# Kernel tuning notes

Measured on AMD Instinct MI355X. Metric: run time of the kernel, lower is better.

The kernel has to match this reference:

```python
import jax, jax.numpy as jnp
import numpy as np

B, T, F, C, D, R = 8, 1000, 96, 16, 64, 4
S = F // R
EPS = 1e-5


def _ln(x, g, b):
    # LayerNorm over last (frequency) dim, matching nn.LayerNorm(fe) on [B,C,T,F]
    m = jnp.mean(x, -1, keepdims=True)
    v = jnp.mean((x - m) ** 2, -1, keepdims=True)
    return (x - m) / jnp.sqrt(v + EPS) * g + b


def _gelu(x):
    return jax.nn.gelu(x, approximate=False)  # torch nn.GELU default (erf)


def setup_inputs() -> dict:
    key = jax.random.key(0)
    ks = jax.random.split(key, 16)
    def nrm(k, shape, fan_in):
        return jax.random.normal(k, shape, jnp.float32) / np.sqrt(fan_in)
    return {
        "input": jax.random.normal(ks[0], (B, 2, T, F), jnp.float32),
        "ln_in_g": jnp.ones((F,), jnp.float32),
        "ln_in_b": jnp.zeros((F,), jnp.float32),
        "w_in": nrm(ks[1], (C, 2), 2),
        "b_in": jnp.zeros((C,), jnp.float32),
        "gru_wx": nrm(ks[2], (3 * C, C), C),   # z|r|n input projections (1x1 conv, no bias)
        "gru_wh": nrm(ks[3], (3 * C, C), C),   # z|r|n hidden projections
        "ln_att_g": jnp.ones((F,), jnp.float32),
        "ln_att_b": jnp.zeros((F,), jnp.float32),
        "wq": nrm(ks[4], (D, C), C),
        "bq": jnp.zeros((D,), jnp.float32),
        "wk": nrm(ks[5], (D, C), C),
        "bk": jnp.zeros((D,), jnp.float32),
        "wv": nrm(ks[6], (D, C), C),
        "bv": jnp.zeros((D,), jnp.float32),
        "wo": nrm(ks[7], (C, D), D),
        "bo": jnp.zeros((C,), jnp.float32),
        "ln_m_g": jnp.ones((F,), jnp.float32),
        "ln_m_b": jnp.zeros((F,), jnp.float32),
        "w_m1": nrm(ks[8], (C, C), C),
        "b_m1": jnp.zeros((C,), jnp.float32),
        "w_m2": nrm(ks[9], (C, C), C),
        "b_m2": jnp.zeros((C,), jnp.float32),
        "ln_out_g": jnp.ones((F,), jnp.float32),
        "ln_out_b": jnp.zeros((F,), jnp.float32),
        "w_out": nrm(ks[10], (2, C), C),
        "b_out": jnp.zeros((2,), jnp.float32),
    }


def _fwd(input, ln_in_g, ln_in_b, w_in, b_in, gru_wx, gru_wh,
         ln_att_g, ln_att_b, wq, bq, wk, bk, wv, bv, wo, bo,
         ln_m_g, ln_m_b, w_m1, b_m1, w_m2, b_m2,
         ln_out_g, ln_out_b, w_out, b_out):
    b = input.shape[0]
    # conv_in: LayerNorm -> 1x1 Conv (2->C) -> GELU
    x = _gelu(jnp.einsum('oc,bctf->botf', w_in, _ln(input, ln_in_g, ln_in_b))
              + b_in[None, :, None, None])  # [B,C,T,F]

    # ConvGRU (kernel 1, no bias): precompute input gates, scan over time
    gx = jnp.einsum('gc,bctf->tbgf', gru_wx, x)  # [T,B,3C,F]
    h0 = jnp.zeros((b, C, F), x.dtype)

    def step(h, gx_t):
        gh = jnp.einsum('gc,bcf->bgf', gru_wh, h)
        zx, rx, nx = jnp.split(gx_t, 3, axis=1)
        zh, rh, nh = jnp.split(gh, 3, axis=1)
        z = jax.nn.sigmoid(zx + zh)
        r = jax.nn.sigmoid(rx + rh)
        n = jnp.tanh(nx + r * nh)
        h = (1.0 - z) * n + z * h
        return h, h

    h_last, hs = jax.lax.scan(step, h0, gx)
    x = x + jnp.moveaxis(hs, 0, 2)  # residual add of GRU output

    # PreNormShortcut(LongShortAttention): local window r + segment-pooled long keys over F
    y = _ln(x, ln_att_g, ln_att_b)
    q = jnp.einsum('dc,bctf->btfd', wq, y) + bq
    k = jnp.einsum('dc,bctf->btfd', wk, y) + bk
    v = jnp.einsum('dc,bctf->btfd', wv, y) + bv
    qs = q.reshape(b, T, S, R, D)
    kk = k.reshape(b, T, S, R, D)
    vv = v.reshape(b, T, S, R, D)
    k_long = kk.mean(3)  # [B,T,S,D]
    v_long = vv.mean(3)
    scale = D ** -0.5
    sc_s = jnp.einsum('btsqd,btskd->btsqk', qs, kk) * scale   # local scores [B,T,S,R,R]
    sc_l = jnp.einsum('btsqd,btmd->btsqm', qs, k_long) * scale  # long scores [B,T,S,R,S]
    a = jax.nn.softmax(jnp.concatenate([sc_s, sc_l], -1), axis=-1)
    o = (jnp.einsum('btsqk,btskd->btsqd', a[..., :R], vv)
         + jnp.einsum('btsqm,btmd->btsqd', a[..., R:], v_long))
    o = o.reshape(b, T, F, D)
    x = x + jnp.einsum('cd,btfd->bctf', wo, o) + bo[None, :, None, None]

    # PreNormShortcut(conv-GELU-conv)
    y = _ln(x, ln_m_g, ln_m_b)
    y = _gelu(jnp.einsum('oc,bctf->botf', w_m1, y) + b_m1[None, :, None, None])
    y = jnp.einsum('oc,bctf->botf', w_m2, y) + b_m2[None, :, None, None]
    x = x + y

    # conv_out: LayerNorm -> 1x1 Conv (C->2) -> Tanh, then outer residual
    y = jnp.tanh(jnp.einsum('oc,bctf->botf', w_out, _ln(x, ln_out_g, ln_out_b))
                 + b_out[None, :, None, None])
    return input + y, h_last


def reference(input, ln_in_g, ln_in_b, w_in, b_in, gru_wx, gru_wh,
              ln_att_g, ln_att_b, wq, bq, wk, bk, wv, bv, wo, bo,
              ln_m_g, ln_m_b, w_m1, b_m1, w_m2, b_m2,
              ln_out_g, ln_out_b, w_out, b_out):
    return _fwd(input, ln_in_g, ln_in_b, w_in, b_in, gru_wx, gru_wh,
                ln_att_g, ln_att_b, wq, bq, wk, bk, wv, bv, wo, bo,
                ln_m_g, ln_m_b, w_m1, b_m1, w_m2, b_m2,
                ln_out_g, ln_out_b, w_out, b_out)
```

## Files before the change

### kernel.cpp

```cpp
#include <hip/hip_runtime.h>
#include <math.h>

#define B_ 8
#define T_ 1000
#define F_ 96
#define C_ 16
#define D_ 64
#define EPS_ 1e-5f
#define CH_ 40

typedef short bfrag8 __attribute__((ext_vector_type(8)));
typedef float facc4 __attribute__((ext_vector_type(4)));
typedef float f2v __attribute__((ext_vector_type(2)));
#define MFMA16 __builtin_amdgcn_mfma_f32_16x16x32_bf16

__device__ __forceinline__ float gelu_erf(float v){
    return 0.5f*v*(1.0f+erff(v*0.70710678118654752440f));
}
__device__ __forceinline__ float dot4(float4 a, float4 b){
    return a.x*b.x + a.y*b.y + a.z*b.z + a.w*b.w;
}
__device__ __forceinline__ float ex2(float x){
    float r; asm("v_exp_f32 %0, %1" : "=v"(r) : "v"(x)); return r;
}
__device__ __forceinline__ float ex2n(float x){
    float r; asm("v_exp_f32 %0, -%1" : "=v"(r) : "v"(x)); return r;
}
__device__ __forceinline__ unsigned short f2bf(float x){
    unsigned int u = __float_as_uint(x);
    return (unsigned short)((u + 0x7fffu + ((u>>16)&1u)) >> 16);
}
__device__ __forceinline__ float bf2f(unsigned short s){
    return __uint_as_float(((unsigned int)s)<<16);
}
__device__ __forceinline__ unsigned int pack2bf(float a, float b){
    return (unsigned int)f2bf(a) | ((unsigned int)f2bf(b)<<16);
}

__global__ __launch_bounds__(128) void k_conv_in(
    const float* __restrict__ in, const float* __restrict__ g, const float* __restrict__ bb,
    const float* __restrict__ w_in, const float* __restrict__ b_in,
    float* __restrict__ x,
    const float* __restrict__ wq, const float* __restrict__ bq,
    const float* __restrict__ wk, const float* __restrict__ bk,
    const float* __restrict__ wv, const float* __restrict__ wo,
    const float* __restrict__ wm1, const float* __restrict__ wm2,
    short* __restrict__ gtb, float* __restrict__ uvw,
    short* __restrict__ wv_bf, short* __restrict__ wo_bf,
    short* __restrict__ wm1_bf, short* __restrict__ wm2_bf)
{
    int bt = blockIdx.x;
    int tid = threadIdx.x;

    if (bt == B_*T_){
        for (int idx = tid; idx < 256; idx += 128){
            int c1 = idx & 15, c2 = idx >> 4;
            float acc = 0.f;
            #pragma unroll 8
            for (int d=0; d<64; ++d)
                acc += wq[d*16 + c1] * wk[d*16 + c2];
            gtb[c2*16 + c1] = (short)f2bf(0.125f * acc);
        }
        if (tid < 16){
            float a = 0.f;
            for (int d=0; d<64; ++d) a += wq[d*16 + tid] * bk[d];
            uvw[tid] = 0.125f * a;
        } else if (tid < 32){
            int cc = tid - 16;
            float a = 0.f;
            for (int d=0; d<64; ++d) a += bq[d] * wk[d*16 + cc];
            uvw[16 + cc] = 0.125f * a;
        } else if (tid == 32){
            float a = 0.f;
            for (int d=0; d<64; ++d) a += bq[d] * bk[d];
            uvw[32] = 0.125f * a;
        }
        for (int i = tid; i < 1024; i += 128){
            wv_bf[i] = (short)f2bf(wv[i]);
            wo_bf[i] = (short)f2bf(wo[i]);
        }
        for (int i = tid; i < 256; i += 128){
            wm1_bf[i] = (short)f2bf(wm1[i]);
            wm2_bf[i] = (short)f2bf(wm2[i]);
        }
        return;
    }

    int b = bt / T_; int t = bt % T_;
    float i0=0.f, i1=0.f;
    size_t base0 = ((size_t)(b*2+0)*T_ + t)*F_;
    size_t base1 = ((size_t)(b*2+1)*T_ + t)*F_;
    if (tid < F_){ i0 = in[base0+tid]; i1 = in[base1+tid]; }
    float s0=i0, q0=i0*i0, s1=i1, q1=i1*i1;
    #pragma unroll
    for (int off=32; off>=1; off>>=1){
        s0 += __shfl_xor(s0, off);
        q0 += __shfl_xor(q0, off);
        s1 += __shfl_xor(s1, off);
        q1 += __shfl_xor(q1, off);
    }
    __shared__ float part[2][4];
    if ((tid & 63) == 0){
        float* p = part[tid>>6];
        p[0]=s0; p[1]=q0; p[2]=s1; p[3]=q1;
    }
    __syncthreads();
    float S0 = part[0][0]+part[1][0];
    float Q0 = part[0][1]+part[1][1];
    float S1 = part[0][2]+part[1][2];
    float Q1 = part[0][3]+part[1][3];
    float m0 = S0*(1.f/F_), m1 = S1*(1.f/F_);
    float ri0 = rsqrtf(Q0*(1.f/F_) - m0*m0 + EPS_);
    float ri1 = rsqrtf(Q1*(1.f/F_) - m1*m1 + EPS_);
    if (tid < F_){
        float gg = g[tid], b0 = bb[tid];
        float y0 = (i0-m0)*ri0*gg + b0;
        float y1 = (i1-m1)*ri1*gg + b0;
        float xv[16];
        #pragma unroll
        for (int c=0;c<C_;++c){
            xv[c] = gelu_erf(w_in[c*2+0]*y0 + w_in[c*2+1]*y1 + b_in[c]);
        }
        float4* xp = (float4*)(x + (((size_t)b*T_+t)*F_ + tid)*C_);
        xp[0] = make_float4(xv[0],xv[1],xv[2],xv[3]);
        xp[1] = make_float4(xv[4],xv[5],xv[6],xv[7]);
        xp[2] = make_float4(xv[8],xv[9],xv[10],xv[11]);
        xp[3] = make_float4(xv[12],xv[13],xv[14],xv[15]);
    }
}

#define DPPF(src, ctrl) __int_as_float(__builtin_amdgcn_update_dpp(0, __float_as_int(src), (ctrl), 0xF, 0xF, false))
#define L2E_ 1.44269504088896340736f

#define GATHER_PAIRDOTS(XV, WZ, WR, WN, SZ, SR, SN) { \
    f2v A0,P2,P7,P5,PF,PD,P8,PA; \
    A0.x = (XV);            A0.y = DPPF((XV),0xB1); \
    P2.x = DPPF(A0.x,0x4E); P2.y = DPPF(A0.y,0x4E); \
    P7.x = DPPF(A0.x,0x141);P7.y = DPPF(A0.y,0x141); \
    P5.x = DPPF(P7.x,0x4E); P5.y = DPPF(P7.y,0x4E); \
    PF.x = DPPF(A0.x,0x140);PF.y = DPPF(A0.y,0x140); \
    PD.x = DPPF(PF.x,0x4E); PD.y = DPPF(PF.y,0x4E); \
    P8.x = DPPF(PF.x,0x141);P8.y = DPPF(PF.y,0x141); \
    PA.x = DPPF(P8.x,0x4E); PA.y = DPPF(P8.y,0x4E); \
    f2v sza = WZ[0]*A0, sra = WR[0]*A0, sna = WN[0]*A0; \
    sza = __builtin_elementwise_fma(WZ[1],P2,sza); \
    sra = __builtin_elementwise_fma(WR[1],P2,sra); \
    sna = __builtin_elementwise_fma(WN[1],P2,sna); \
    sza = __builtin_elementwise_fma(WZ[2],P7,sza); \
    sra = __builtin_elementwise_fma(WR[2],P7,sra); \
    sna = __builtin_elementwise_fma(WN[2],P7,sna); \
    sza = __builtin_elementwise_fma(WZ[3],P5,sza); \
    sra = __builtin_elementwise_fma(WR[3],P5,sra); \
    sna = __builtin_elementwise_fma(WN[3],P5,sna); \
    f2v szb = WZ[4]*PF, srb = WR[4]*PF, snb = WN[4]*PF; \
    szb = __builtin_elementwise_fma(WZ[5],PD,szb); \
    srb = __builtin_elementwise_fma(WR[5],PD,srb); \
    snb = __builtin_elementwise_fma(WN[5],PD,snb); \
    szb = __builtin_elementwise_fma(WZ[6],P8,szb); \
    srb = __builtin_elementwise_fma(WR[6],P8,srb); \
    snb = __builtin_elementwise_fma(WN[6],P8,snb); \
    szb = __builtin_elementwise_fma(WZ[7],PA,szb); \
    srb = __builtin_elementwise_fma(WR[7],PA,srb); \
    snb = __builtin_elementwise_fma(WN[7],PA,snb); \
    SZ = sza + szb; SR = sra + srb; SN = sna + snb; \
}

__global__ __launch_bounds__(256, 1) void k_gru(
    const float* __restrict__ x, const float* __restrict__ wx, const float* __restrict__ wh,
    float* __restrict__ hs, float* __restrict__ d_out)
{
    int blk = blockIdx.x;
    int b = blk / 24, f0 = (blk % 24) * 4;
    int tid = threadIdx.x;
    int wave = tid >> 6, lane = tid & 63;
    int c = lane & 15, ch = lane >> 4;
    int f = f0 + ch;

    __shared__ float GG[2][(CH_+1)*192];

    const int pm0[8] = {0,2,7,5,15,13,8,10};
    const int pm1[8] = {1,3,6,4,14,12,9,11};

    if (wave != 0){
        float4 Wxz[4], Wxr[4], Wxn[4];
        #pragma unroll
        for (int q=0;q<4;++q){
            float4 az = *(const float4*)(wx + ( 0+c)*16 + 4*q);
            float4 ar = *(const float4*)(wx + (16+c)*16 + 4*q);
            float4 an = *(const float4*)(wx + (32+c)*16 + 4*q);
            Wxz[q] = make_float4(az.x*L2E_, az.y*L2E_, az.z*L2E_, az.w*L2E_);
            Wxr[q] = make_float4(ar.x*L2E_, ar.y*L2E_, ar.z*L2E_, ar.w*L2E_);
            Wxn[q] = make_float4(an.x*2.f*L2E_, an.y*2.f*L2E_, an.z*2.f*L2E_, an.w*2.f*L2E_);
        }
        const float* gb0 = x + (size_t)b*T_*(F_*C_) + f*C_;
        const int tl0 = (wave-1)*14;
        const int tl1 = (tl0 + 14 < CH_) ? tl0 + 14 : CH_;
        #define PRODUCE(K, BF) { \
            _Pragma("unroll 2") \
            for (int tl=tl0; tl<tl1; ++tl){ \
                const float* xp2 = gb0 + (size_t)((K)*CH_ + tl)*(F_*C_); \
                float4 x0 = *(const float4*)(xp2 + 0); \
                float4 x1 = *(const float4*)(xp2 + 4); \
                float4 x2 = *(const float4*)(xp2 + 8); \
                float4 x3 = *(const float4*)(xp2 + 12); \
                float zx = dot4(Wxz[0],x0)+dot4(Wxz[1],x1)+dot4(Wxz[2],x2)+dot4(Wxz[3],x3); \
                float rx = dot4(Wxr[0],x0)+dot4(Wxr[1],x1)+dot4(Wxr[2],x2)+dot4(Wxr[3],x3); \
                float nx = dot4(Wxn[0],x0)+dot4(Wxn[1],x1)+dot4(Wxn[2],x2)+dot4(Wxn[3],x3); \
                float* gq = &GG[BF][tl*192 + lane]; \
                gq[0] = zx; gq[64] = rx; gq[128] = nx; \
            } }
        PRODUCE(0, 0);
        __syncthreads();
        for (int k=0; k<T_/CH_; ++k){
            if (k+1 < T_/CH_){
                if ((k+1)&1){ PRODUCE(k+1, 1); } else { PRODUCE(k+1, 0); }
            }
            __syncthreads();
        }
        #undef PRODUCE
    } else {
        __builtin_amdgcn_s_setprio(1);
        f2v Wz[8], Wr[8], Wn[8];
        #pragma unroll
        for (int j=0;j<8;++j){
            int ka = c ^ pm0[j], kb = c ^ pm1[j];
            Wz[j].x = L2E_*wh[( 0+c)*16 + ka];      Wz[j].y = L2E_*wh[( 0+c)*16 + kb];
            Wr[j].x = L2E_*wh[(16+c)*16 + ka];      Wr[j].y = L2E_*wh[(16+c)*16 + kb];
            Wn[j].x = 2.f*L2E_*wh[(32+c)*16 + ka];  Wn[j].y = 2.f*L2E_*wh[(32+c)*16 + kb];
        }
        float hc = 0.f;
        size_t hsb = (size_t)b*T_*(F_*C_) + f0*C_ + lane;
        __syncthreads();
        for (int k=0; k<T_/CH_; ++k){
            const float* gp = GG[k&1];
            float gzv = gp[lane], grv = gp[64+lane], gnv = gp[128+lane];
            #pragma unroll 8
            for (int tl=0; tl<CH_; ++tl){
                const float* np = gp + (tl+1)*192 + lane;
                float gzn = np[0], grn = np[64], gnn = np[128];
                f2v SZ, SR, SN;
                GATHER_PAIRDOTS(hc, Wz, Wr, Wn, SZ, SR, SN);
                float z = __builtin_amdgcn_rcpf(1.f + ex2n(gzv + (SZ.x + SZ.y)));
                float r = __builtin_amdgcn_rcpf(1.f + ex2n(grv + (SR.x + SR.y)));
                float u = __builtin_amdgcn_rcpf(1.f + ex2(fmaf(r, SN.x + SN.y, gnv)));
                float n = fmaf(-2.f, u, 1.f);
                hc = n + z*(hc - n);
                hs[hsb + (size_t)(k*CH_ + tl)*(F_*C_)] = hc;
                gzv = gzn; grv = grn; gnv = gnn;
            }
            __syncthreads();
        }
        d_out[(size_t)B_*2*T_*F_ + ((size_t)b*C_ + c)*F_ + f] = hc;
    }
}

#define XR_FL   0
#define YB_SH   3072
#define YGB_SH  5376
#define PG_SH   3072
#define YMB_SH  7680
#define E_FL    4224
#define GL_FL   4320
#define GM_FL   4416
#define VBT_SH  8880
#define VLBT_SH 15024
#define SC_FL   8536
#define OB_SH   17072
#define PL_SH   23216
#define GTB_SH  17072
#define UU_FL   8728
#define VV_FL   8744
#define W0_FL   8760
#define OSC_FL  8776
#define MEA_FL  9288
#define RST_FL  9304
#define TOTF    13144

__device__ __forceinline__ void ln_stats16(float* S, int tid){
    int c = tid & 15, g = tid >> 4;
    float s=0.f, q=0.f;
    #pragma unroll
    for (int i=0;i<6;++i){
        float v = S[XR_FL + (g*6+i)*16 + c];
        s += v; q += v*v;
    }
    S[OSC_FL + g*16 + c] = s;
    S[OSC_FL + 256 + g*16 + c] = q;
    __syncthreads();
    if (tid < 16){
        float Sm=0.f, Q=0.f;
        #pragma unroll
        for (int g2=0; g2<16; ++g2){
            Sm += S[OSC_FL + g2*16 + tid];
            Q  += S[OSC_FL + 256 + g2*16 + tid];
        }
        float m = Sm*(1.f/96.f);
        S[MEA_FL+tid] = m;
        S[RST_FL+tid] = rsqrtf(Q*(1.f/96.f) - m*m + EPS_);
    }
    __syncthreads();
}

__global__ __launch_bounds__(256) void k_tail(
    const float* __restrict__ x, const float* __restrict__ hs, const float* __restrict__ input,
    const float* __restrict__ ln_att_g, const float* __restrict__ ln_att_b,
    const short* __restrict__ gtb, const float* __restrict__ uvw,
    const short* __restrict__ wv_bf, const float* __restrict__ bv,
    const short* __restrict__ wo_bf, const float* __restrict__ bo,
    const float* __restrict__ ln_m_g, const float* __restrict__ ln_m_b,
    const short* __restrict__ wm1_bf, const float* __restrict__ bm1,
    const short* __restrict__ wm2_bf, const float* __restrict__ bm2,
    const float* __restrict__ ln_o_g, const float* __restrict__ ln_o_b,
    const float* __restrict__ w_out, const float* __restrict__ b_out,
    float* __restrict__ out)
{
    int bt = blockIdx.x; int b = bt / T_; int t = bt % T_;
    int tid = threadIdx.x;
    int w = tid >> 6, lane = tid & 63;
    int n = lane & 15, q2 = lane >> 4;
    __shared__ float S[TOTF];
    short* Ssh = (short*)S;
    const bfrag8 ZF = {0,0,0,0,0,0,0,0};
    const int svl = (n >> 1) & 3;
    const int swo = n & 7;

    size_t xbase = ((size_t)b*T_ + t)*(size_t)(F_*C_);

    {
        const float4* xg = (const float4*)(x + xbase);
        const float4* hg = (const float4*)(hs + xbase);
        float4* XR4 = (float4*)(S + XR_FL);
        for (int i4 = tid; i4 < 384; i4 += 256){
            float4 a = xg[i4], h = hg[i4];
            XR4[i4] = make_float4(a.x+h.x, a.y+h.y, a.z+h.z, a.w+h.w);
        }
        if (tid < 64){
            int cc2 = tid >> 2, c1g = (tid & 3)*4;
            *(uint2*)(Ssh + GTB_SH + cc2*24 + c1g) = *(const uint2*)(gtb + cc2*16 + c1g);
        } else if (tid < 97){
            S[UU_FL + (tid - 64)] = uvw[tid - 64];
        }
    }
    bfrag8 Bv = ZF, Bm1 = ZF, Bm2 = ZF;
    if (q2 < 2){
        Bv  = *(const bfrag8*)(wv_bf  + (16*w + n)*16 + q2*8);
        Bm1 = *(const bfrag8*)(wm1_bf + n*16 + q2*8);
        Bm2 = *(const bfrag8*)(wm2_bf + n*16 + q2*8);
    }
    bfrag8 Bo0 = *(const bfrag8*)(wo_bf + n*64 + q2*8);
    bfrag8 Bo1 = *(const bfrag8*)(wo_bf + n*64 + 32 + q2*8);
    float bvr  = bv[16*w + n];
    float bor  = bo[n];
    float bm1r = bm1[n];
    float bm2r = bm2[n];
    __syncthreads();

    ln_stats16(S, tid);

    {
        float4* XR4 = (float4*)(S + XR_FL);
        for (int i4 = tid; i4 < 384; i4 += 256){
            int f = i4 >> 2, c4 = i4 & 3;
            float4 v = XR4[i4];
            float4 m4 = *(float4*)(S + MEA_FL + 4*c4);
            float4 r4 = *(float4*)(S + RST_FL + 4*c4);
            float gg = ln_att_g[f], b2 = ln_att_b[f];
            float y0 = (v.x - m4.x)*r4.x*gg + b2;
            float y1 = (v.y - m4.y)*r4.y*gg + b2;
            float y2 = (v.z - m4.z)*r4.z*gg + b2;
            float y3 = (v.w - m4.w)*r4.w*gg + b2;
            uint2 pk = make_uint2(pack2bf(y0,y1), pack2bf(y2,y3));
            *(uint2*)(Ssh + YB_SH + f*24 + c4*4) = pk;
        }
    }
    __syncthreads();

    if (tid < 96){
        int f = tid;
        float yv[16];
        uint4 u0 = *(const uint4*)(Ssh + YB_SH + f*24);
        uint4 u1 = *(const uint4*)(Ssh + YB_SH + f*24 + 8);
        unsigned int uu[8] = {u0.x,u0.y,u0.z,u0.w,u1.x,u1.y,u1.z,u1.w};
        #pragma unroll
        for (int j=0;j<8;++j){
            yv[2*j]   = bf2f((unsigned short)(uu[j] & 0xffff));
            yv[2*j+1] = bf2f((unsigned short)(uu[j] >> 16));
        }
        float de = 0.f, dg = 0.f;
        #pragma unroll
        for (int cc=0; cc<16; ++cc){
            de += yv[cc]*S[UU_FL+cc];
            dg += yv[cc]*S[VV_FL+cc];
        }
        S[E_FL + f]  = de + S[W0_FL];
        S[GL_FL + f] = dg;
    }
    for (int e = tid; e < 384; e += 256){
        int m = e >> 4, cc = e & 15;
        float sm = bf2f((unsigned short)Ssh[YB_SH + (4*m+0)*24 + cc])
                 + bf2f((unsigned short)Ssh[YB_SH + (4*m+1)*24 + cc])
                 + bf2f((unsigned short)Ssh[YB_SH + (4*m+2)*24 + cc])
                 + bf2f((unsigned short)Ssh[YB_SH + (4*m+3)*24 + cc]);
        Ssh[YMB_SH + m*24 + cc] = (short)f2bf(0.25f*sm);
    }
    if (tid < 128){
        int row = 24 + (tid >> 4), cc = tid & 15;
        Ssh[YMB_SH + row*24 + cc] = 0;
    }
    __syncthreads();

    {
        #pragma unroll
        for (int mt=0; mt<6; ++mt){
            bfrag8 A = ZF;
            if (q2 < 2) A = *(const bfrag8*)(Ssh + YB_SH + (mt*16 + n)*24 + q2*8);
            facc4 acc = {bvr, bvr, bvr, bvr};
            acc = MFMA16(A, Bv, acc, 0, 0, 0);
            uint2 pk = make_uint2(pack2bf(acc[0],acc[1]), pack2bf(acc[2],acc[3]));
            int g = 2*mt + (q2>>1);
            *(uint2*)(Ssh + VBT_SH + (16*w + n)*96 + ((g^svl)<<3) + ((q2&1)<<2)) = pk;
        }
        #pragma unroll
        for (int mt=0; mt<2; ++mt){
            bfrag8 A = ZF;
            if (q2 < 2) A = *(const bfrag8*)(Ssh + YMB_SH + (mt*16 + n)*24 + q2*8);
            facc4 acc = {bvr, bvr, bvr, bvr};
            acc = MFMA16(A, Bv, acc, 0, 0, 0);
            uint2 pk = make_uint2(pack2bf(acc[0],acc[1]), pack2bf(acc[2],acc[3]));
            int g = 2*mt + (q2>>1);
            *(uint2*)(Ssh + VLBT_SH + (16*w + n)*32 + ((g^svl)<<3) + ((q2&1)<<2)) = pk;
        }
        bfrag8 Bg = ZF;
        if (q2 < 2) Bg = *(const bfrag8*)(Ssh + GTB_SH + n*24 + q2*8);
        for (int mt = w; mt < 6; mt += 4){
            bfrag8 A = ZF;
            if (q2 < 2) A = *(const bfrag8*)(Ssh + YB_SH + (mt*16 + n)*24 + q2*8);
            facc4 acc = {0.f,0.f,0.f,0.f};
            acc = MFMA16(A, Bg, acc, 0, 0, 0);
            #pragma unroll
            for (int r=0;r<4;++r)
                Ssh[YGB_SH + (mt*16 + q2*4 + r)*24 + n] = (short)f2bf(acc[r]);
        }
        if (tid >= 224 && tid < 248){
            int m = tid - 224;
            float a2 = 0.f;
            #pragma unroll
            for (int cc=0; cc<16; ++cc)
                a2 += bf2f((unsigned short)Ssh[YMB_SH + m*24 + cc]) * S[VV_FL + cc];
            S[GM_FL + m] = a2;
        }
    }
    __syncthreads();

    for (int j = w; j < 18; j += 4){
        int mt = j / 3, kind = j % 3;
        bfrag8 A = ZF;
        if (q2 < 2) A = *(const bfrag8*)(Ssh + YGB_SH + (mt*16 + n)*24 + q2*8);
        bfrag8 Bf = ZF;
        if (kind == 0){
            if (q2 < 2) Bf = *(const bfrag8*)(Ssh + YB_SH + (mt*16 + n)*24 + q2*8);
        } else {
            int nt = kind - 1;
            if (q2 < 2) Bf = *(const bfrag8*)(Ssh + YMB_SH + (nt*16 + n)*24 + q2*8);
        }
        facc4 acc = {0.f,0.f,0.f,0.f};
        acc = MFMA16(A, Bf, acc, 0, 0, 0);
        if (kind == 0){
            if ((n >> 2) == q2){
                #pragma unroll
                for (int r=0;r<4;++r)
                    S[SC_FL + (mt*16 + q2*4 + r)*29 + (n & 3)] = acc[r];
            }
        } else {
            int nt = kind - 1;
            if (!(nt == 1 && n >= 8)){
                #pragma unroll
                for (int r=0;r<4;++r)
                    S[SC_FL + (mt*16 + q2*4 + r)*29 + 4 + nt*16 + n] = acc[r];
            }
        }
    }
    __syncthreads();

    if (tid < 96){
        int f = tid;
        int lsq = (f >> 2) & 3;
        float e_ = S[E_FL + f];
        const float* row = S + SC_FL + f*29;
        float sl[4];
        #pragma unroll
        for (int j=0;j<4;++j)
            sl[j] = row[j] + e_ + S[GL_FL + (f & ~3) + j];
        float sg[24];
        #pragma unroll
        for (int m=0;m<24;++m)
            sg[m] = row[4 + m] + e_ + S[GM_FL + m];
        float mx = sl[0];
        #pragma unroll
        for (int j=1;j<4;++j) mx = fmaxf(mx, sl[j]);
        #pragma unroll
        for (int m=0;m<24;++m) mx = fmaxf(mx, sg[m]);
        float sum = 0.f;
        #pragma unroll
        for (int j=0;j<4;++j){ sl[j] = __expf(sl[j]-mx); sum += sl[j]; }
        #pragma unroll
        for (int m=0;m<24;++m){ sg[m] = __expf(sg[m]-mx); sum += sg[m]; }
        float inv = __builtin_amdgcn_rcpf(sum);
        unsigned int lo = pack2bf(sl[0]*inv, sl[1]*inv);
        unsigned int hi = pack2bf(sl[2]*inv, sl[3]*inv);
        uint4 z4 = make_uint4(0u,0u,0u,0u);
        uint4 p0 = make_uint4(lsq==0?lo:0u, lsq==0?hi:0u, lsq==1?lo:0u, lsq==1?hi:0u);
        uint4 p1 = make_uint4(lsq==2?lo:0u, lsq==2?hi:0u, lsq==3?lo:0u, lsq==3?hi:0u);
        uint4* plp = (uint4*)(Ssh + PL_SH + f*32);
        int swp = (f >> 1) & 3;
        plp[0^swp] = p0; plp[1^swp] = p1; plp[2^swp] = z4; plp[3^swp] = z4;
        unsigned int gdw[12];
        #pragma unroll
        for (int m=0;m<12;++m) gdw[m] = pack2bf(sg[2*m]*inv, sg[2*m+1]*inv);
        uint4* pgp = (uint4*)(Ssh + PG_SH + f*48);
        pgp[0] = make_uint4(gdw[0],gdw[1],gdw[2],gdw[3]);
        pgp[1] = make_uint4(gdw[4],gdw[5],gdw[6],gdw[7]);
        pgp[2] = make_uint4(gdw[8],gdw[9],gdw[10],gdw[11]);
        pgp[3] = z4;
    }
    __syncthreads();

    {
        bfrag8 Avl = *(const bfrag8*)(Ssh + VLBT_SH + (16*w + n)*32 + ((q2^svl)<<3));
        #pragma unroll
        for (int nt=0; nt<6; ++nt){
            bfrag8 Avb = *(const bfrag8*)(Ssh + VBT_SH + (16*w + n)*96 + (((2*nt + q2)^svl)<<3));
            bfrag8 Bpl = *(const bfrag8*)(Ssh + PL_SH + (nt*16 + n)*32 + ((q2^svl)<<3));
            bfrag8 Bpg = *(const bfrag8*)(Ssh + PG_SH + (nt*16 + n)*48 + q2*8);
            facc4 acc = {0.f,0.f,0.f,0.f};
            acc = MFMA16(Avb, Bpl, acc, 0, 0, 0);
            acc = MFMA16(Avl, Bpg, acc, 0, 0, 0);
            uint2 pk = make_uint2(pack2bf(acc[0],acc[1]), pack2bf(acc[2],acc[3]));
            int go = 2*w + (q2>>1);
            *(uint2*)(Ssh + OB_SH + (nt*16 + n)*64 + ((go^swo)<<3) + ((q2&1)<<2)) = pk;
        }
    }
    __syncthreads();

    for (int mt = w; mt < 6; mt += 4){
        bfrag8 A0 = *(const bfrag8*)(Ssh + OB_SH + (mt*16 + n)*64 + ((q2^swo)<<3));
        bfrag8 A1 = *(const bfrag8*)(Ssh + OB_SH + (mt*16 + n)*64 + (((4+q2)^swo)<<3));
        facc4 acc = {bor, bor, bor, bor};
        acc = MFMA16(A0, Bo0, acc, 0, 0, 0);
        acc = MFMA16(A1, Bo1, acc, 0, 0, 0);
        #pragma unroll
        for (int r=0;r<4;++r)
            S[XR_FL + (mt*16 + q2*4 + r)*16 + n] += acc[r];
    }
    __syncthreads();

    ln_stats16(S, tid);
    {
        float4* XR4 = (float4*)(S + XR_FL);
        for (int i4 = tid; i4 < 384; i4 += 256){
            int f = i4 >> 2, c4 = i4 & 3;
            float4 v = XR4[i4];
            float4 m4 = *(float4*)(S + MEA_FL + 4*c4);
            float4 r4 = *(float4*)(S + RST_FL + 4*c4);
            float gg = ln_m_g[f], b2 = ln_m_b[f];
            float y0 = (v.x - m4.x)*r4.x*gg + b2;
            float y1 = (v.y - m4.y)*r4.y*gg + b2;
            float y2 = (v.z - m4.z)*r4.z*gg + b2;
            float y3 = (v.w - m4.w)*r4.w*gg + b2;
            uint2 pk = make_uint2(pack2bf(y0,y1), pack2bf(y2,y3));
            *(uint2*)(Ssh + YB_SH + f*24 + c4*4) = pk;
        }
    }
    __syncthreads();
    for (int mt = w; mt < 6; mt += 4){
        bfrag8 A = ZF;
        if (q2 < 2) A = *(const bfrag8*)(Ssh + YB_SH + (mt*16 + n)*24 + q2*8);
        facc4 acc = {bm1r, bm1r, bm1r, bm1r};
        acc = MFMA16(A, Bm1, acc, 0, 0, 0);
        #pragma unroll
        for (int r=0;r<4;++r)
            Ssh[YGB_SH + (mt*16 + q2*4 + r)*24 + n] = (short)f2bf(gelu_erf(acc[r]));
    }
    __syncthreads();
    for (int mt = w; mt < 6; mt += 4){
        bfrag8 A = ZF;
        if (q2 < 2) A = *(const bfrag8*)(Ssh + YGB_SH + (mt*16 + n)*24 + q2*8);
        facc4 acc = {bm2r, bm2r, bm2r, bm2r};
        acc = MFMA16(A, Bm2, acc, 0, 0, 0);
        #pragma unroll
        for (int r=0;r<4;++r)
            S[XR_FL + (mt*16 + q2*4 + r)*16 + n] += acc[r];
    }
    __syncthreads();

    ln_stats16(S, tid);
    if (tid < 192){
        int ch = tid >= 96, f = tid - 96*ch;
        float gg = ln_o_g[f], b2 = ln_o_b[f];
        float acc = b_out[ch];
        float4* XR4 = (float4*)(S + XR_FL);
        #pragma unroll
        for (int c4=0;c4<4;++c4){
            float4 x4 = XR4[f*4 + c4];
            float4 m4 = *(float4*)(S + MEA_FL + 4*c4);
            float4 r4 = *(float4*)(S + RST_FL + 4*c4);
            float4 w4 = *(const float4*)(w_out + ch*16 + 4*c4);
            float4 tm;
            tm.x = (x4.x - m4.x)*r4.x*gg + b2;
            tm.y = (x4.y - m4.y)*r4.y*gg + b2;
            tm.z = (x4.z - m4.z)*r4.z*gg + b2;
            tm.w = (x4.w - m4.w)*r4.w*gg + b2;
            acc += dot4(w4, tm);
        }
        size_t oidx = ((size_t)(b*2+ch)*T_ + t)*F_ + f;
        out[oidx] = input[oidx] + tanhf(acc);
    }
}

extern "C" void kernel_launch(void* const* d_in, const int* in_sizes, int n_in,
                              void* d_out, int out_size, void* d_ws, size_t ws_size,
                              hipStream_t stream)
{
    const float* input   = (const float*)d_in[0];
    const float* ln_in_g = (const float*)d_in[1];
    const float* ln_in_b = (const float*)d_in[2];
    const float* w_in    = (const float*)d_in[3];
    const float* b_in    = (const float*)d_in[4];
    const float* gru_wx  = (const float*)d_in[5];
    const float* gru_wh  = (const float*)d_in[6];
    const float* ln_att_g= (const float*)d_in[7];
    const float* ln_att_b= (const float*)d_in[8];
    const float* wq = (const float*)d_in[9];
    const float* bq = (const float*)d_in[10];
    const float* wk = (const float*)d_in[11];
    const float* bk = (const float*)d_in[12];
    const float* wv = (const float*)d_in[13];
    const float* bv = (const float*)d_in[14];
    const float* wo = (const float*)d_in[15];
    const float* bo = (const float*)d_in[16];
    const float* ln_m_g = (const float*)d_in[17];
    const float* ln_m_b = (const float*)d_in[18];
    const float* w_m1 = (const float*)d_in[19];
    const float* b_m1 = (const float*)d_in[20];
    const float* w_m2 = (const float*)d_in[21];
    const float* b_m2 = (const float*)d_in[22];
    const float* ln_out_g = (const float*)d_in[23];
    const float* ln_out_b = (const float*)d_in[24];
    const float* w_out = (const float*)d_in[25];
    const float* b_out = (const float*)d_in[26];
    float* out = (float*)d_out;

    const size_t NX = (size_t)B_*T_*F_*C_;
    float* x   = (float*)d_ws;
    float* hs  = x + NX;
    float* uvw = x + 2*NX;
    short* wv_bf  = (short*)(x + 2*NX + 64);
    short* wo_bf  = wv_bf + 1024;
    short* wm1_bf = wo_bf + 1024;
    short* wm2_bf = wm1_bf + 256;
    short* gtb    = wm2_bf + 256;

    k_conv_in<<<B_*T_ + 1, 128, 0, stream>>>(input, ln_in_g, ln_in_b, w_in, b_in, x,
        wq, bq, wk, bk, wv, wo, w_m1, w_m2,
        gtb, uvw, wv_bf, wo_bf, wm1_bf, wm2_bf);
    k_gru<<<192, 256, 0, stream>>>(x, gru_wx, gru_wh, hs, out);
    k_tail<<<B_*T_, 256, 0, stream>>>(x, hs, input, ln_att_g, ln_att_b,
        gtb, uvw, wv_bf, bv, wo_bf, bo, ln_m_g, ln_m_b, wm1_bf, b_m1, wm2_bf, b_m2,
        ln_out_g, ln_out_b, w_out, b_out, out);
}
```

Measured before the change: 430.5 us.

## Fuse GRU and tail kernels into time-quartered launches overlapping recurrence with tail

Merges the GRU recurrence and the per-timestep tail into one kernel, launched in four time quarters. Each launch runs 192 GRU blocks for the next quarter next to tail blocks for the previous quarter, so the serial recurrence overlaps the parallel tail work. The GRU hidden state is carried between launches through a workspace buffer, and the chunk size shrinks so it reuses the tail's shared memory. The costs are extra launches, a workspace read and write of the state, and GRU blocks competing with tail blocks for compute units. Ordering depends on the stream serialising the launches.

```diff
diff --git a/kernel.cpp b/kernel.cpp
--- a/kernel.cpp
+++ b/kernel.cpp
@@ -7,7 +7,9 @@
 #define C_ 16
 #define D_ 64
 #define EPS_ 1e-5f
-#define CH_ 40
+#define CH_ 25
+#define QT_ 250
+#define NKC_ 10
 
 typedef short bfrag8 __attribute__((ext_vector_type(8)));
 typedef float facc4 __attribute__((ext_vector_type(4)));
@@ -131,6 +133,7 @@
 
 #define DPPF(src, ctrl) __int_as_float(__builtin_amdgcn_update_dpp(0, __float_as_int(src), (ctrl), 0xF, 0xF, false))
 #define L2E_ 1.44269504088896340736f
+#define GGROW ((CH_+1)*192)
 
 #define GATHER_PAIRDOTS(XV, WZ, WR, WN, SZ, SR, SN) { \
     f2v A0,P2,P7,P5,PF,PD,P8,PA; \
@@ -165,95 +168,6 @@
     SZ = sza + szb; SR = sra + srb; SN = sna + snb; \
 }
 
-__global__ __launch_bounds__(256, 1) void k_gru(
-    const float* __restrict__ x, const float* __restrict__ wx, const float* __restrict__ wh,
-    float* __restrict__ hs, float* __restrict__ d_out)
-{
-    int blk = blockIdx.x;
-    int b = blk / 24, f0 = (blk % 24) * 4;
-    int tid = threadIdx.x;
-    int wave = tid >> 6, lane = tid & 63;
-    int c = lane & 15, ch = lane >> 4;
-    int f = f0 + ch;
-
-    __shared__ float GG[2][(CH_+1)*192];
-
-    const int pm0[8] = {0,2,7,5,15,13,8,10};
-    const int pm1[8] = {1,3,6,4,14,12,9,11};
-
-    if (wave != 0){
-        float4 Wxz[4], Wxr[4], Wxn[4];
-        #pragma unroll
-        for (int q=0;q<4;++q){
-            float4 az = *(const float4*)(wx + ( 0+c)*16 + 4*q);
-            float4 ar = *(const float4*)(wx + (16+c)*16 + 4*q);
-            float4 an = *(const float4*)(wx + (32+c)*16 + 4*q);
-            Wxz[q] = make_float4(az.x*L2E_, az.y*L2E_, az.z*L2E_, az.w*L2E_);
-            Wxr[q] = make_float4(ar.x*L2E_, ar.y*L2E_, ar.z*L2E_, ar.w*L2E_);
-            Wxn[q] = make_float4(an.x*2.f*L2E_, an.y*2.f*L2E_, an.z*2.f*L2E_, an.w*2.f*L2E_);
-        }
-        const float* gb0 = x + (size_t)b*T_*(F_*C_) + f*C_;
-        const int tl0 = (wave-1)*14;
-        const int tl1 = (tl0 + 14 < CH_) ? tl0 + 14 : CH_;
-        #define PRODUCE(K, BF) { \
-            _Pragma("unroll 2") \
-            for (int tl=tl0; tl<tl1; ++tl){ \
-                const float* xp2 = gb0 + (size_t)((K)*CH_ + tl)*(F_*C_); \
-                float4 x0 = *(const float4*)(xp2 + 0); \
-                float4 x1 = *(const float4*)(xp2 + 4); \
-                float4 x2 = *(const float4*)(xp2 + 8); \
-                float4 x3 = *(const float4*)(xp2 + 12); \
-                float zx = dot4(Wxz[0],x0)+dot4(Wxz[1],x1)+dot4(Wxz[2],x2)+dot4(Wxz[3],x3); \
-                float rx = dot4(Wxr[0],x0)+dot4(Wxr[1],x1)+dot4(Wxr[2],x2)+dot4(Wxr[3],x3); \
-                float nx = dot4(Wxn[0],x0)+dot4(Wxn[1],x1)+dot4(Wxn[2],x2)+dot4(Wxn[3],x3); \
-                float* gq = &GG[BF][tl*192 + lane]; \
-                gq[0] = zx; gq[64] = rx; gq[128] = nx; \
-            } }
-        PRODUCE(0, 0);
-        __syncthreads();
-        for (int k=0; k<T_/CH_; ++k){
-            if (k+1 < T_/CH_){
-                if ((k+1)&1){ PRODUCE(k+1, 1); } else { PRODUCE(k+1, 0); }
-            }
-            __syncthreads();
-        }
-        #undef PRODUCE
-    } else {
-        __builtin_amdgcn_s_setprio(1);
-        f2v Wz[8], Wr[8], Wn[8];
-        #pragma unroll
-        for (int j=0;j<8;++j){
-            int ka = c ^ pm0[j], kb = c ^ pm1[j];
-            Wz[j].x = L2E_*wh[( 0+c)*16 + ka];      Wz[j].y = L2E_*wh[( 0+c)*16 + kb];
-            Wr[j].x = L2E_*wh[(16+c)*16 + ka];      Wr[j].y = L2E_*wh[(16+c)*16 + kb];
-            Wn[j].x = 2.f*L2E_*wh[(32+c)*16 + ka];  Wn[j].y = 2.f*L2E_*wh[(32+c)*16 + kb];
-        }
-        float hc = 0.f;
-        size_t hsb = (size_t)b*T_*(F_*C_) + f0*C_ + lane;
-        __syncthreads();
-        for (int k=0; k<T_/CH_; ++k){
-            const float* gp = GG[k&1];
-            float gzv = gp[lane], grv = gp[64+lane], gnv = gp[128+lane];
-            #pragma unroll 8
-            for (int tl=0; tl<CH_; ++tl){
-                const float* np = gp + (tl+1)*192 + lane;
-                float gzn = np[0], grn = np[64], gnn = np[128];
-                f2v SZ, SR, SN;
-                GATHER_PAIRDOTS(hc, Wz, Wr, Wn, SZ, SR, SN);
-                float z = __builtin_amdgcn_rcpf(1.f + ex2n(gzv + (SZ.x + SZ.y)));
-                float r = __builtin_amdgcn_rcpf(1.f + ex2n(grv + (SR.x + SR.y)));
-                float u = __builtin_amdgcn_rcpf(1.f + ex2(fmaf(r, SN.x + SN.y, gnv)));
-                float n = fmaf(-2.f, u, 1.f);
-                hc = n + z*(hc - n);
-                hs[hsb + (size_t)(k*CH_ + tl)*(F_*C_)] = hc;
-                gzv = gzn; grv = grn; gnv = gnn;
-            }
-            __syncthreads();
-        }
-        d_out[(size_t)B_*2*T_*F_ + ((size_t)b*C_ + c)*F_ + f] = hc;
-    }
-}
-
 #define XR_FL   0
 #define YB_SH   3072
 #define YGB_SH  5376
@@ -301,8 +215,10 @@
     __syncthreads();
 }
 
-__global__ __launch_bounds__(256) void k_tail(
-    const float* __restrict__ x, const float* __restrict__ hs, const float* __restrict__ input,
+__global__ __launch_bounds__(256, 1) void k_mid(
+    const float* __restrict__ x, const float* __restrict__ wx, const float* __restrict__ wh,
+    float* __restrict__ hs, float* __restrict__ hstate, float* __restrict__ d_out,
+    const float* __restrict__ input,
     const float* __restrict__ ln_att_g, const float* __restrict__ ln_att_b,
     const short* __restrict__ gtb, const float* __restrict__ uvw,
     const short* __restrict__ wv_bf, const float* __restrict__ bv,
@@ -312,13 +228,107 @@
     const short* __restrict__ wm2_bf, const float* __restrict__ bm2,
     const float* __restrict__ ln_o_g, const float* __restrict__ ln_o_b,
     const float* __restrict__ w_out, const float* __restrict__ b_out,
-    float* __restrict__ out)
+    float* __restrict__ out,
+    int gru_t0, int gru_on, int tail_t0, int tail_nt)
 {
-    int bt = blockIdx.x; int b = bt / T_; int t = bt % T_;
+    __shared__ float S[TOTF];
     int tid = threadIdx.x;
+    int nGru = gru_on ? 192 : 0;
+
+    if ((int)blockIdx.x < nGru){
+        float* GG0 = S;
+        float* GG1 = S + GGROW;
+        int blk = blockIdx.x;
+        int b = blk / 24, f0 = (blk % 24) * 4;
+        int wave = tid >> 6, lane = tid & 63;
+        int c = lane & 15, ch = lane >> 4;
+        int f = f0 + ch;
+        const int k0 = gru_t0 / CH_;
+
+        const int pm0[8] = {0,2,7,5,15,13,8,10};
+        const int pm1[8] = {1,3,6,4,14,12,9,11};
+
+        if (wave != 0){
+            float4 Wxz[4], Wxr[4], Wxn[4];
+            #pragma unroll
+            for (int q=0;q<4;++q){
+                float4 az = *(const float4*)(wx + ( 0+c)*16 + 4*q);
+                float4 ar = *(const float4*)(wx + (16+c)*16 + 4*q);
+                float4 an = *(const float4*)(wx + (32+c)*16 + 4*q);
+                Wxz[q] = make_float4(az.x*L2E_, az.y*L2E_, az.z*L2E_, az.w*L2E_);
+                Wxr[q] = make_float4(ar.x*L2E_, ar.y*L2E_, ar.z*L2E_, ar.w*L2E_);
+                Wxn[q] = make_float4(an.x*2.f*L2E_, an.y*2.f*L2E_, an.z*2.f*L2E_, an.w*2.f*L2E_);
+            }
+            const float* gb0 = x + (size_t)b*T_*(F_*C_) + f*C_;
+            const int tl0 = (wave-1)*9;
+            const int tl1 = (tl0 + 9 < CH_) ? tl0 + 9 : CH_;
+            #define PRODUCE(K, GP) { \
+                _Pragma("unroll 3") \
+                for (int tl=tl0; tl<tl1; ++tl){ \
+                    const float* xp2 = gb0 + (size_t)((K)*CH_ + tl)*(F_*C_); \
+                    float4 x0 = *(const float4*)(xp2 + 0); \
+                    float4 x1 = *(const float4*)(xp2 + 4); \
+                    float4 x2 = *(const float4*)(xp2 + 8); \
+                    float4 x3 = *(const float4*)(xp2 + 12); \
+                    float zx = dot4(Wxz[0],x0)+dot4(Wxz[1],x1)+dot4(Wxz[2],x2)+dot4(Wxz[3],x3); \
+                    float rx = dot4(Wxr[0],x0)+dot4(Wxr[1],x1)+dot4(Wxr[2],x2)+dot4(Wxr[3],x3); \
+                    float nx = dot4(Wxn[0],x0)+dot4(Wxn[1],x1)+dot4(Wxn[2],x2)+dot4(Wxn[3],x3); \
+                    float* gq = (GP) + tl*192 + lane; \
+                    gq[0] = zx; gq[64] = rx; gq[128] = nx; \
+                } }
+            PRODUCE(k0, GG0);
+            __syncthreads();
+            for (int kk=0; kk<NKC_; ++kk){
+                if (kk+1 < NKC_){
+                    if ((kk+1)&1){ PRODUCE(k0+kk+1, GG1); } else { PRODUCE(k0+kk+1, GG0); }
+                }
+                __syncthreads();
+            }
+            #undef PRODUCE
+        } else {
+            __builtin_amdgcn_s_setprio(1);
+            f2v Wz[8], Wr[8], Wn[8];
+            #pragma unroll
+            for (int j=0;j<8;++j){
+                int ka = c ^ pm0[j], kb = c ^ pm1[j];
+                Wz[j].x = L2E_*wh[( 0+c)*16 + ka];      Wz[j].y = L2E_*wh[( 0+c)*16 + kb];
+                Wr[j].x = L2E_*wh[(16+c)*16 + ka];      Wr[j].y = L2E_*wh[(16+c)*16 + kb];
+                Wn[j].x = 2.f*L2E_*wh[(32+c)*16 + ka];  Wn[j].y = 2.f*L2E_*wh[(32+c)*16 + kb];
+            }
+            float hc = (gru_t0 == 0) ? 0.f : hstate[blk*64 + lane];
+            size_t hsb = (size_t)b*T_*(F_*C_) + f0*C_ + lane;
+            __syncthreads();
+            for (int kk=0; kk<NKC_; ++kk){
+                const float* gp = (kk&1) ? GG1 : GG0;
+                float gzv = gp[lane], grv = gp[64+lane], gnv = gp[128+lane];
+                #pragma unroll 5
+                for (int tl=0; tl<CH_; ++tl){
+                    const float* np = gp + (tl+1)*192 + lane;
+                    float gzn = np[0], grn = np[64], gnn = np[128];
+                    f2v SZ, SR, SN;
+                    GATHER_PAIRDOTS(hc, Wz, Wr, Wn, SZ, SR, SN);
+                    float z = __builtin_amdgcn_rcpf(1.f + ex2n(gzv + (SZ.x + SZ.y)));
+                    float r = __builtin_amdgcn_rcpf(1.f + ex2n(grv + (SR.x + SR.y)));
+                    float u = __builtin_amdgcn_rcpf(1.f + ex2(fmaf(r, SN.x + SN.y, gnv)));
+                    float n = fmaf(-2.f, u, 1.f);
+                    hc = n + z*(hc - n);
+                    hs[hsb + (size_t)((k0+kk)*CH_ + tl)*(F_*C_)] = hc;
+                    gzv = gzn; grv = grn; gnv = gnn;
+                }
+                __syncthreads();
+            }
+            hstate[blk*64 + lane] = hc;
+            if (gru_t0 + QT_ == T_)
+                d_out[(size_t)B_*2*T_*F_ + ((size_t)b*C_ + c)*F_ + f] = hc;
+        }
+        return;
+    }
+
+    int idx = blockIdx.x - nGru;
+    int b = idx / tail_nt;
+    int t = tail_t0 + idx % tail_nt;
     int w = tid >> 6, lane = tid & 63;
     int n = lane & 15, q2 = lane >> 4;
-    __shared__ float S[TOTF];
     short* Ssh = (short*)S;
     const bfrag8 ZF = {0,0,0,0,0,0,0,0};
     const int svl = (n >> 1) & 3;
@@ -659,12 +669,19 @@
     short* wm1_bf = wo_bf + 1024;
     short* wm2_bf = wm1_bf + 256;
     short* gtb    = wm2_bf + 256;
+    float* hstate = (float*)(gtb + 256);
 
     k_conv_in<<<B_*T_ + 1, 128, 0, stream>>>(input, ln_in_g, ln_in_b, w_in, b_in, x,
         wq, bq, wk, bk, wv, wo, w_m1, w_m2,
         gtb, uvw, wv_bf, wo_bf, wm1_bf, wm2_bf);
-    k_gru<<<192, 256, 0, stream>>>(x, gru_wx, gru_wh, hs, out);
-    k_tail<<<B_*T_, 256, 0, stream>>>(x, hs, input, ln_att_g, ln_att_b,
-        gtb, uvw, wv_bf, bv, wo_bf, bo, ln_m_g, ln_m_b, wm1_bf, b_m1, wm2_bf, b_m2,
-        ln_out_g, ln_out_b, w_out, b_out, out);
-}
+
+    #define MIDARGS x, gru_wx, gru_wh, hs, hstate, out, input, ln_att_g, ln_att_b, \
+        gtb, uvw, wv_bf, bv, wo_bf, bo, ln_m_g, ln_m_b, wm1_bf, b_m1, wm2_bf, b_m2, \
+        ln_out_g, ln_out_b, w_out, b_out, out
+    k_mid<<<192,          256, 0, stream>>>(MIDARGS,   0, 1,   0,   0);
+    k_mid<<<192 + 8*QT_,  256, 0, stream>>>(MIDARGS, 250, 1,   0, QT_);
+    k_mid<<<192 + 8*QT_,  256, 0, stream>>>(MIDARGS, 500, 1, 250, QT_);
+    k_mid<<<192 + 8*QT_,  256, 0, stream>>>(MIDARGS, 750, 1, 500, QT_);
+    k_mid<<<8*QT_,        256, 0, stream>>>(MIDARGS,   0, 0, 750, QT_);
+    #undef MIDARGS
+}
```

Measured after the change: 442.6 us. 2.8% more time.
